# Kernel optimization log

Hardware: AMD Instinct MI355X
Metric: run time of the kernel (lower is better)

## Reference

```python
import jax, jax.numpy as jnp
import numpy as np

B, S, W, MODES, NUM, NLAYERS = 32, 8192, 128, 16, 8, 4
LG = 8192 + 40 - 1  # szie + len - 1 (Gabor filter length)
PI = float(np.pi)


def setup_inputs() -> dict:
    key = jax.random.key(0)
    ks = jax.random.split(key, 10)
    scale = 1.0 / (W * W)
    return {
        "x": jax.random.normal(ks[0], (B, S, 1), jnp.float32),
        "w1_re": scale * jax.random.uniform(ks[1], (NLAYERS, W, W, MODES), jnp.float32),
        "w1_im": scale * jax.random.uniform(ks[2], (NLAYERS, W, W, MODES), jnp.float32),
        "gamma": jnp.tile(jnp.linspace(0.01, 0.02, NUM, dtype=jnp.float32)[None], (NLAYERS, 1)),
        "fwhm": jnp.tile(jnp.linspace(0.001, 0.002, NUM, dtype=jnp.float32)[None], (NLAYERS, 1)),
        "w2": jax.random.uniform(ks[3], (NLAYERS, NUM), jnp.float32),
        "cw": jax.random.normal(ks[4], (NLAYERS, W, W), jnp.float32) / np.sqrt(W),
        "cb": jnp.zeros((NLAYERS, W), jnp.float32),
        "fc0_w": jax.random.normal(ks[5], (W, 2), jnp.float32) / np.sqrt(2.0),
        "fc0_b": jnp.zeros((W,), jnp.float32),
        "fc1_w": jax.random.normal(ks[6], (128, W), jnp.float32) / np.sqrt(W),
        "fc1_b": jnp.zeros((128,), jnp.float32),
        "fc2_w": jax.random.normal(ks[7], (1, 128), jnp.float32) / np.sqrt(128.0),
        "fc2_b": jnp.zeros((1,), jnp.float32),
    }


def _spectral_conv(h, w_re, w_im, gamma, fwhm, w2):
    # h: [B, C, S] real. w_re/w_im: [C, C, MODES]. gamma/fwhm/w2: [NUM].
    u = jnp.linspace(-0.5, 0.5, LG, dtype=h.dtype)                      # [LG]
    t1 = (gamma * PI / (fwhm + 1e-5))[:, None]                          # [NUM,1]
    gab = jnp.exp(-(t1 ** 2) * (u[None, :] - fwhm[:, None]) ** 2)       # [NUM,LG]
    gab = jnp.fft.ifftshift(gab, axes=-1)[:, :MODES]                     # [NUM,MODES]
    # weights2 is a scalar per latent kernel -> fold the num-reduction into an
    # effective per-mode Gabor weight (exact same math as the repeated einsum + sum).
    g_eff = jnp.einsum("k,km->m", w2, gab)                               # [MODES]
    w1 = (w_re + 1j * w_im) * g_eff[None, None, :]                       # [C,C,MODES] complex
    xf = jnp.fft.rfft(h)                                                 # [B,C,F], F=S//2+1
    out_m = jnp.einsum("bim,iom->bom", xf[..., :MODES], w1)              # [B,C,MODES]
    out = jnp.zeros(xf.shape, dtype=xf.dtype).at[..., :MODES].set(out_m)
    return jnp.fft.irfft(out, n=h.shape[-1])                             # [B,C,S]


def reference(x, w1_re, w1_im, gamma, fwhm, w2, cw, cb, fc0_w, fc0_b, fc1_w, fc1_b, fc2_w, fc2_b):
    b, s, _ = x.shape
    grid = jnp.broadcast_to(jnp.linspace(0.0, 1.0, s, dtype=x.dtype)[None, :, None], (b, s, 1))
    h = jnp.concatenate([x, grid], axis=-1)                              # [B,S,2]
    h = h @ fc0_w.T + fc0_b                                              # [B,S,W]
    h = jnp.transpose(h, (0, 2, 1))                                      # [B,W,S]
    for l in range(NLAYERS):
        x1 = _spectral_conv(h, w1_re[l], w1_im[l], gamma[l], fwhm[l], w2[l])
        x2 = jnp.einsum("oi,bis->bos", cw[l], h) + cb[l][None, :, None]  # 1x1 conv
        h = x1 + x2
        if l < NLAYERS - 1:
            h = jax.nn.gelu(h, approximate=False)
    h = jnp.transpose(h, (0, 2, 1))                                      # [B,S,W]
    h = jax.nn.gelu(h @ fc1_w.T + fc1_b, approximate=False)              # [B,S,128]
    return h @ fc2_w.T + fc2_b                                           # [B,S,1]
```

## Files before the change

kernel.cpp:

```cpp
#include <hip/hip_runtime.h>
#include <hip/hip_fp16.h>

#define BB 32
#define SS 8192
#define CC 128
#define MM 16
#define NUMK 8
#define NL 4

#define TWO_PI 6.2831853071795864769f

typedef _Float16 f16x8 __attribute__((ext_vector_type(8)));
typedef float f32x4 __attribute__((ext_vector_type(4)));

#define MFMA16(a, b, c) __builtin_amdgcn_mfma_f32_16x16x32_f16((a), (b), (c), 0, 0, 0)

__device__ __forceinline__ float gelu_f(float v) {
    float u = 0.7978845608f * fmaf(0.044715f * v * v, v, v);
    float a = fabsf(u);
    float e = __expf(-2.0f * a);
    float th = __fdividef(1.0f - e, 1.0f + e);
    th = copysignf(th, u);
    return 0.5f * v * (1.0f + th);
}

__device__ __align__(256) __half g_trigA[SS * 32];
__device__ __align__(256) __half g_trigD[32 * SS];
__device__ __align__(256) __half g_cwh[NL * CC * CC];
__device__ __align__(256) __half g_fc1h[CC * CC];
__device__ __align__(256) __half g_omh[BB * CC * 32];
__device__ __align__(256) float  g_Xfp[BB * 64 * 32 * CC];
__device__ __align__(256) float  g_Xf[BB * 32 * CC];
__device__ __align__(256) float  g_Xx[BB * MM * 2];
__device__ __align__(256) float  g_Xg[MM * 2];

__global__ __launch_bounds__(256) void k_prep(const float* __restrict__ cw,
                                              const float* __restrict__ fc1_w) {
    int idx = blockIdx.x * 256 + threadIdx.x;
    if (idx < NL * CC * CC) g_cwh[idx] = __float2half(cw[idx]);
    if (idx < CC * CC)      g_fc1h[idx] = __float2half(fc1_w[idx]);
}

__global__ __launch_bounds__(256) void k_trig() {
    int s = blockIdx.x * 256 + threadIdx.x;
    for (int m = 0; m < MM; m++) {
        int ms = (m * s) & (SS - 1);
        float th = (float)ms * (TWO_PI / (float)SS);
        float sn, cs;
        sincosf(th, &sn, &cs);
        g_trigA[s * 32 + m]        = __float2half(cs);
        g_trigA[s * 32 + 16 + m]   = __float2half(sn);
        g_trigD[m * SS + s]        = __float2half(cs);
        g_trigD[(16 + m) * SS + s] = __float2half(-sn);
    }
}

__global__ __launch_bounds__(256) void k_dftx(const float* __restrict__ x) {
    __shared__ float red[4][MM][2];
    int blk = blockIdx.x;
    int t = threadIdx.x;
    int lane = t & 63;
    int wv = t >> 6;

    float accR[MM], accI[MM], cr[MM], ci[MM], pc[MM], ps[MM];
#pragma unroll
    for (int m = 0; m < MM; m++) {
        float sn, cs;
        sincosf((TWO_PI / (float)SS) * (float)(m * t), &sn, &cs);
        cr[m] = cs; ci[m] = -sn;
        sincosf((TWO_PI * 256.0f / (float)SS) * (float)m, &sn, &cs);
        pc[m] = cs; ps[m] = -sn;
        accR[m] = 0.f; accI[m] = 0.f;
    }
    for (int k = 0; k < 32; k++) {
        int s = t + (k << 8);
        float v = (blk < BB) ? x[(blk << 13) + s] : (float)s * (1.0f / 8191.0f);
#pragma unroll
        for (int m = 0; m < MM; m++) {
            accR[m] = fmaf(v, cr[m], accR[m]);
            accI[m] = fmaf(v, ci[m], accI[m]);
            float nc = cr[m] * pc[m] - ci[m] * ps[m];
            float ns = cr[m] * ps[m] + ci[m] * pc[m];
            cr[m] = nc; ci[m] = ns;
        }
    }
#pragma unroll
    for (int m = 0; m < MM; m++) {
#pragma unroll
        for (int off = 32; off > 0; off >>= 1) {
            accR[m] += __shfl_xor(accR[m], off, 64);
            accI[m] += __shfl_xor(accI[m], off, 64);
        }
        if (lane == 0) { red[wv][m][0] = accR[m]; red[wv][m][1] = accI[m]; }
    }
    __syncthreads();
    if (t < MM * 2) {
        int m = t >> 1, p = t & 1;
        float s = red[0][m][p] + red[1][m][p] + red[2][m][p] + red[3][m][p];
        if (blk < BB) g_Xx[(blk << 5) + (m << 1) + p] = s;
        else          g_Xg[(m << 1) + p] = s;
    }
}

__global__ __launch_bounds__(256) void k_xf0(const float* __restrict__ fc0_w,
                                             const float* __restrict__ fc0_b) {
    int n = blockIdx.x * 256 + threadIdx.x;
    int i = n & 127, m2 = (n >> 7) & 31, b = n >> 12;
    int m = m2 & 15, p = m2 >> 4;
    float xv = g_Xx[(b << 5) + (m << 1) + p];
    float gv = g_Xg[(m << 1) + p];
    float v = fc0_w[2 * i] * xv + fc0_w[2 * i + 1] * gv;
    if (p == 0 && m == 0) v += (float)SS * fc0_b[i];
    g_Xf[(b << 12) + (m2 << 7) + i] = v;
}

__global__ __launch_bounds__(256) void k_fc0(const float* __restrict__ x,
                                             const float* __restrict__ fc0_w,
                                             const float* __restrict__ fc0_b,
                                             __half* __restrict__ h) {
    int idx = blockIdx.x * 256 + threadIdx.x;
    int wq = idx & 15;
    int s = (idx >> 4) & (SS - 1);
    int b = idx >> 17;
    float g = (float)s * (1.0f / (float)(SS - 1));
    float xv = x[(b << 13) + s];
    union { __half2 q[4]; f16x8 v; } pk;
#pragma unroll
    for (int j = 0; j < 4; j++) {
        int w = wq * 8 + j * 2;
        float4 fw = *(const float4*)(fc0_w + 2 * w);
        float2 fb = *(const float2*)(fc0_b + w);
        float v0 = fmaf(fw.x, xv, fmaf(fw.y, g, fb.x));
        float v1 = fmaf(fw.z, xv, fmaf(fw.w, g, fb.y));
        pk.q[j] = __floats2half2_rn(v0, v1);
    }
    *(f16x8*)((char*)h + ((long)idx << 4)) = pk.v;
}

__global__ __launch_bounds__(256) void k_red2() {
    int n = blockIdx.x * 256 + threadIdx.x;
    int i = n & 127, m2 = (n >> 7) & 31, b = n >> 12;
    const float* p = g_Xfp + (((b << 6) << 5) + (m2 << 7)) + i;
    float s = 0.f;
#pragma unroll 8
    for (int t = 0; t < 64; t++) s += p[t << 12];
    g_Xf[(b << 12) + (m2 << 7) + i] = s;
}

__global__ __launch_bounds__(256) void k_mix(const float* __restrict__ w1_re,
                                             const float* __restrict__ w1_im,
                                             const float* __restrict__ gamma,
                                             const float* __restrict__ fwhm,
                                             const float* __restrict__ w2,
                                             const float* __restrict__ cb, int l) {
    __shared__ float geff[MM];
    int t = threadIdx.x;
    if (t < MM) {
        float g = 0.f;
        for (int k = 0; k < NUMK; k++) {
            float fw = fwhm[l * NUMK + k];
            float t1 = gamma[l * NUMK + k] * 3.14159265358979f / (fw + 1e-5f);
            float u = (float)t * (1.0f / 8230.0f) - fw;
            g = fmaf(w2[l * NUMK + k], expf(-t1 * t1 * u * u), g);
        }
        geff[t] = g;
    }
    __syncthreads();

    int n = blockIdx.x * 256 + t;
    int m = n & 15, o = (n >> 4) & 127, b = n >> 11;
    const float* xr = g_Xf + (b << 12) + (m << 7);
    const float* xi = g_Xf + (b << 12) + ((16 + m) << 7);
    const float* wr = w1_re + (l << 18) + (o << 4) + m;
    const float* wi = w1_im + (l << 18) + (o << 4) + m;
    float orr = 0.f, oii = 0.f;
    for (int i = 0; i < CC; i++) {
        float xrv = xr[i], xiv = xi[i];
        float wrv = wr[i << 11], wiv = wi[i << 11];
        orr = fmaf(xrv, wrv, orr); orr = fmaf(-xiv, wiv, orr);
        oii = fmaf(xrv, wiv, oii); oii = fmaf(xiv, wrv, oii);
    }
    float sc = geff[m] * (2.0f / (float)SS) * ((m == 0) ? 0.5f : 1.0f);
    float base = (m == 0) ? cb[l * CC + o] : 0.0f;
    g_omh[(b << 12) + (o << 5) + m]      = __float2half(orr * sc + base);
    g_omh[(b << 12) + (o << 5) + 16 + m] = __float2half(-oii * sc);
}

#define GEMM_STEP(KS, HA, HB)                                                       \
    _Pragma("unroll")                                                               \
    for (int af = 0; af < 8; af++) {                                                \
        int row = (af << 4) + lr;                                                   \
        const f16x8 av = *(const f16x8*)(ldsA + (row << 8) +                        \
                          ((((KS << 2) + lg) ^ (row & 7)) << 4));                   \
        acc[af][0] = MFMA16(av, HA, acc[af][0]);                                    \
        acc[af][1] = MFMA16(av, HB, acc[af][1]);                                    \
    }

#define LOAD_HF(S0X)                                                                \
    {                                                                               \
        int hr = (((b << 13) + (S0X) + (wid << 5) + lr) << 8) + (lg << 4);          \
        hf0 = *(const f16x8*)(h_c + hr);                                            \
        hf1 = *(const f16x8*)(h_c + hr + (16 << 8));                                \
        hf2 = *(const f16x8*)(h_c + hr + (1 << 6));                                 \
        hf3 = *(const f16x8*)(h_c + hr + (16 << 8) + (1 << 6));                     \
        hf4 = *(const f16x8*)(h_c + hr + (2 << 6));                                 \
        hf5 = *(const f16x8*)(h_c + hr + (16 << 8) + (2 << 6));                     \
        hf6 = *(const f16x8*)(h_c + hr + (3 << 6));                                 \
        hf7 = *(const f16x8*)(h_c + hr + (16 << 8) + (3 << 6));                     \
    }

#define LOAD_TF(S0X)                                                                \
    {                                                                               \
        int tr2 = (((S0X) + (wid << 5) + lr) << 6) + (lg << 4);                     \
        tf0 = *(const f16x8*)(ta_c + tr2);                                          \
        tf1 = *(const f16x8*)(ta_c + tr2 + (16 << 6));                              \
    }

__global__ __launch_bounds__(256, 2) void k_layer(__half* __restrict__ h, int l) {
    __shared__ __align__(16) char smem[73728];
    char* ldsA = smem;
    char* ldsO = smem + 32768;
    char* ldsS = smem + 40960;
    int bi = blockIdx.x;
    int b = bi >> 4, grp = bi & 15;
    int Sg = grp << 9;
    int t = threadIdx.x;
    int wid = __builtin_amdgcn_readfirstlane(t >> 6);
    int l6 = t & 63, lr = l6 & 15, lg = l6 >> 4;
    const char* h_c = (const char*)h;
    char* hw = (char*)h;
    const char* cw_c = (const char*)(g_cwh + l * CC * CC);
    const char* om_c = (const char*)(g_omh + (b << 12));
    const char* ta_c = (const char*)g_trigA;
    const char* td_c = (const char*)g_trigD;
    char* strip = ldsS + (wid << 13);

#pragma unroll
    for (int k = 0; k < 8; k++) {
        int c = (k << 8) + t;
        f16x8 v = *(const f16x8*)(cw_c + (c << 4));
        int row = c >> 4, c16 = c & 15;
        *(f16x8*)(ldsA + (row << 8) + ((c16 ^ (row & 7)) << 4)) = v;
    }
#pragma unroll
    for (int k = 0; k < 2; k++) {
        int c = (k << 8) + t;
        f16x8 v = *(const f16x8*)(om_c + (c << 4));
        int row = c >> 2, c4 = c & 3;
        *(f16x8*)(ldsO + (row << 6) + ((c4 ^ (row & 3)) << 4)) = v;
    }
    f16x8 hf0, hf1, hf2, hf3, hf4, hf5, hf6, hf7, tf0, tf1;
    LOAD_HF(Sg)
    LOAD_TF(Sg)
    __syncthreads();

    f32x4 dacc[8][2];
#pragma unroll
    for (int af = 0; af < 8; af++) {
        dacc[af][0] = (f32x4){0.f, 0.f, 0.f, 0.f};
        dacc[af][1] = (f32x4){0.f, 0.f, 0.f, 0.f};
    }

    for (int ti = 0; ti < 4; ti++) {
        int S0 = Sg + (ti << 7);
        f32x4 acc[8][2];
#pragma unroll
        for (int af = 0; af < 8; af++) {
            acc[af][0] = (f32x4){0.f, 0.f, 0.f, 0.f};
            acc[af][1] = (f32x4){0.f, 0.f, 0.f, 0.f};
        }
        __builtin_amdgcn_s_setprio(1);
        GEMM_STEP(0, hf0, hf1)
        GEMM_STEP(1, hf2, hf3)
        GEMM_STEP(2, hf4, hf5)
        GEMM_STEP(3, hf6, hf7)
#pragma unroll
        for (int af = 0; af < 8; af++) {
            int row = (af << 4) + lr;
            const f16x8 ov = *(const f16x8*)(ldsO + (row << 6) + ((lg ^ (row & 3)) << 4));
            acc[af][0] = MFMA16(ov, tf0, acc[af][0]);
            acc[af][1] = MFMA16(ov, tf1, acc[af][1]);
        }
        __builtin_amdgcn_s_setprio(0);
        if (ti < 3) {
            int S0n = S0 + 128;
            LOAD_HF(S0n)
            LOAD_TF(S0n)
        }
        f16x8 td0, td1;
        {
            int sgl = S0 + (wid << 5) + (lg << 3);
            td0 = *(const f16x8*)(td_c + (((lr << 13) + sgl) << 1));
            td1 = *(const f16x8*)(td_c + ((((16 + lr) << 13) + sgl) << 1));
        }
#pragma unroll
        for (int bf = 0; bf < 2; bf++) {
            int s_w = (bf << 4) + lr;
#pragma unroll
            for (int af = 0; af < 8; af++) {
                int o0 = (af << 4) + (lg << 2);
                float v0 = gelu_f(acc[af][bf][0]), v1 = gelu_f(acc[af][bf][1]);
                float v2 = gelu_f(acc[af][bf][2]), v3 = gelu_f(acc[af][bf][3]);
                union { __half2 q[2]; unsigned long long u; } pk;
                pk.q[0] = __floats2half2_rn(v0, v1);
                pk.q[1] = __floats2half2_rn(v2, v3);
                int byte = (s_w << 8) + ((o0 << 1) ^ ((s_w & 15) << 4));
                *(unsigned long long*)(strip + byte) = pk.u;
            }
        }
        asm volatile("s_waitcnt lgkmcnt(0)" ::: "memory");
        __builtin_amdgcn_sched_barrier(0);
#pragma unroll
        for (int af = 0; af < 8; af++) {
            int o = (af << 4) + lr;
            union { unsigned int u[4]; f16x8 v; } bb;
#pragma unroll
            for (int p = 0; p < 4; p++) {
                int s0 = (lg << 3) + 2 * p, s1 = s0 + 1;
                unsigned int lo = *(const unsigned short*)
                    (strip + (s0 << 8) + ((o << 1) ^ ((s0 & 15) << 4)));
                unsigned int hi = *(const unsigned short*)
                    (strip + (s1 << 8) + ((o << 1) ^ ((s1 & 15) << 4)));
                bb.u[p] = lo | (hi << 16);
            }
            dacc[af][0] = MFMA16(td0, bb.v, dacc[af][0]);
            dacc[af][1] = MFMA16(td1, bb.v, dacc[af][1]);
        }
#pragma unroll
        for (int rg = 0; rg < 8; rg++) {
            int s_w = (rg << 2) + lg;
            f16x8 rd = *(const f16x8*)(strip + (s_w << 8) + ((lr ^ (s_w & 15)) << 4));
            *(f16x8*)(hw + (((b << 13) + S0 + (wid << 5) + s_w) << 8) + (lr << 4)) = rd;
        }
    }
    {
        float* xp = g_Xfp + (((b << 6) + (grp << 2) + wid) << 12);
#pragma unroll
        for (int af = 0; af < 8; af++)
#pragma unroll
            for (int mh = 0; mh < 2; mh++)
#pragma unroll
                for (int reg = 0; reg < 4; reg++) {
                    int m2 = (mh << 4) + (lg << 2) + reg;
                    int o = (af << 4) + lr;
                    xp[(m2 << 7) + o] = dacc[af][mh][reg];
                }
    }
}

__global__ __launch_bounds__(256, 2) void k_tail(const __half* __restrict__ h,
                                                 const float* __restrict__ fc1_b,
                                                 const float* __restrict__ fc2_w,
                                                 const float* __restrict__ fc2_b,
                                                 float* __restrict__ out) {
    __shared__ __align__(16) char smem[73728];
    char* ldsA = smem;
    char* ldsO = smem + 32768;
    char* ldsS = smem + 40960;
    int bi = blockIdx.x;
    int b = bi >> 4, grp = bi & 15;
    int Sg = grp << 9;
    int t = threadIdx.x;
    int wid = __builtin_amdgcn_readfirstlane(t >> 6);
    int l6 = t & 63, lr = l6 & 15, lg = l6 >> 4;
    const char* h_c = (const char*)h;
    const char* cw_c = (const char*)(g_cwh + 3 * CC * CC);
    const char* om_c = (const char*)(g_omh + (b << 12));
    const char* ta_c = (const char*)g_trigA;
    const char* f1_c = (const char*)g_fc1h;
    char* strip = ldsS + (wid << 13);

#pragma unroll
    for (int k = 0; k < 8; k++) {
        int c = (k << 8) + t;
        f16x8 v = *(const f16x8*)(cw_c + (c << 4));
        int row = c >> 4, c16 = c & 15;
        *(f16x8*)(ldsA + (row << 8) + ((c16 ^ (row & 7)) << 4)) = v;
    }
#pragma unroll
    for (int k = 0; k < 2; k++) {
        int c = (k << 8) + t;
        f16x8 v = *(const f16x8*)(om_c + (c << 4));
        int row = c >> 2, c4 = c & 3;
        *(f16x8*)(ldsO + (row << 6) + ((c4 ^ (row & 3)) << 4)) = v;
    }
    f16x8 hf0, hf1, hf2, hf3, hf4, hf5, hf6, hf7, tf0, tf1;
    LOAD_HF(Sg)
    LOAD_TF(Sg)
    __syncthreads();

    float f2b = fc2_b[0];
    for (int ti = 0; ti < 4; ti++) {
        int S0 = Sg + (ti << 7);
        {
            f32x4 acc[8][2];
#pragma unroll
            for (int af = 0; af < 8; af++) {
                acc[af][0] = (f32x4){0.f, 0.f, 0.f, 0.f};
                acc[af][1] = (f32x4){0.f, 0.f, 0.f, 0.f};
            }
            __builtin_amdgcn_s_setprio(1);
            GEMM_STEP(0, hf0, hf1)
            GEMM_STEP(1, hf2, hf3)
            GEMM_STEP(2, hf4, hf5)
            GEMM_STEP(3, hf6, hf7)
#pragma unroll
            for (int af = 0; af < 8; af++) {
                int row = (af << 4) + lr;
                const f16x8 ov = *(const f16x8*)(ldsO + (row << 6) + ((lg ^ (row & 3)) << 4));
                acc[af][0] = MFMA16(ov, tf0, acc[af][0]);
                acc[af][1] = MFMA16(ov, tf1, acc[af][1]);
            }
            __builtin_amdgcn_s_setprio(0);
            if (ti < 3) {
                int S0n = S0 + 128;
                LOAD_HF(S0n)
                LOAD_TF(S0n)
            }
#pragma unroll
            for (int bf = 0; bf < 2; bf++) {
                int s_w = (bf << 4) + lr;
#pragma unroll
                for (int af = 0; af < 8; af++) {
                    int o0 = (af << 4) + (lg << 2);
                    union { __half2 q[2]; unsigned long long u; } pk;
                    pk.q[0] = __floats2half2_rn(acc[af][bf][0], acc[af][bf][1]);
                    pk.q[1] = __floats2half2_rn(acc[af][bf][2], acc[af][bf][3]);
                    int byte = (s_w << 8) + ((o0 << 1) ^ ((s_w & 15) << 4));
                    *(unsigned long long*)(strip + byte) = pk.u;
                }
            }
        }
        asm volatile("s_waitcnt lgkmcnt(0)" ::: "memory");
        __builtin_amdgcn_sched_barrier(0);
        {
            f32x4 acc2[8][2];
#pragma unroll
            for (int af = 0; af < 8; af++) {
                acc2[af][0] = (f32x4){0.f, 0.f, 0.f, 0.f};
                acc2[af][1] = (f32x4){0.f, 0.f, 0.f, 0.f};
            }
#pragma unroll
            for (int ks = 0; ks < 4; ks++) {
#pragma unroll
                for (int bf = 0; bf < 2; bf++) {
                    int s_loc = (bf << 4) + lr;
                    union { unsigned int u[4]; f16x8 v; } bb;
#pragma unroll
                    for (int p = 0; p < 4; p++) {
                        int o0 = (ks << 5) + (lg << 3) + 2 * p, o1 = o0 + 1;
                        unsigned int lo = *(const unsigned short*)
                            (strip + (s_loc << 8) + ((o0 << 1) ^ ((s_loc & 15) << 4)));
                        unsigned int hi = *(const unsigned short*)
                            (strip + (s_loc << 8) + ((o1 << 1) ^ ((s_loc & 15) << 4)));
                        bb.u[p] = lo | (hi << 16);
                    }
#pragma unroll
                    for (int af = 0; af < 8; af++) {
                        const f16x8 av = *(const f16x8*)
                            (f1_c + (((af << 4) + lr) << 8) + (ks << 6) + (lg << 4));
                        acc2[af][bf] = MFMA16(av, bb.v, acc2[af][bf]);
                    }
                }
            }
            float p[2] = {0.f, 0.f};
#pragma unroll
            for (int af = 0; af < 8; af++) {
                float4 fb = *(const float4*)(fc1_b + (af << 4) + (lg << 2));
                float4 f2 = *(const float4*)(fc2_w + (af << 4) + (lg << 2));
#pragma unroll
                for (int bf = 0; bf < 2; bf++) {
                    float v0 = gelu_f(acc2[af][bf][0] + fb.x);
                    float v1 = gelu_f(acc2[af][bf][1] + fb.y);
                    float v2 = gelu_f(acc2[af][bf][2] + fb.z);
                    float v3 = gelu_f(acc2[af][bf][3] + fb.w);
                    p[bf] += f2.x * v0 + f2.y * v1 + f2.z * v2 + f2.w * v3;
                }
            }
#pragma unroll
            for (int bf = 0; bf < 2; bf++) {
                float v = p[bf];
                v += __shfl_xor(v, 16, 64);
                v += __shfl_xor(v, 32, 64);
                if (lg == 0) out[(b << 13) + S0 + (wid << 5) + (bf << 4) + lr] = v + f2b;
            }
        }
    }
}

extern "C" void kernel_launch(void* const* d_in, const int* in_sizes, int n_in,
                              void* d_out, int out_size, void* d_ws, size_t ws_size,
                              hipStream_t stream) {
    const float* x      = (const float*)d_in[0];
    const float* w1_re  = (const float*)d_in[1];
    const float* w1_im  = (const float*)d_in[2];
    const float* gamma  = (const float*)d_in[3];
    const float* fwhm   = (const float*)d_in[4];
    const float* w2     = (const float*)d_in[5];
    const float* cw     = (const float*)d_in[6];
    const float* cb     = (const float*)d_in[7];
    const float* fc0_w  = (const float*)d_in[8];
    const float* fc0_b  = (const float*)d_in[9];
    const float* fc1_w  = (const float*)d_in[10];
    const float* fc1_b  = (const float*)d_in[11];
    const float* fc2_w  = (const float*)d_in[12];
    const float* fc2_b  = (const float*)d_in[13];
    float* out = (float*)d_out;

    __half* h = (__half*)d_ws;

    k_prep<<<dim3(256), dim3(256), 0, stream>>>(cw, fc1_w);
    k_trig<<<dim3(32), dim3(256), 0, stream>>>();
    k_dftx<<<dim3(33), dim3(256), 0, stream>>>(x);
    k_xf0<<<dim3(512), dim3(256), 0, stream>>>(fc0_w, fc0_b);
    k_fc0<<<dim3(16384), dim3(256), 0, stream>>>(x, fc0_w, fc0_b, h);
    for (int l = 0; l < NL; l++) {
        k_mix<<<dim3(256), dim3(256), 0, stream>>>(w1_re, w1_im, gamma, fwhm, w2, cb, l);
        if (l < NL - 1) {
            k_layer<<<dim3(512), dim3(256), 0, stream>>>(h, l);
            k_red2<<<dim3(512), dim3(256), 0, stream>>>();
        } else {
            k_tail<<<dim3(512), dim3(256), 0, stream>>>(h, fc1_b, fc2_w, fc2_b, out);
        }
    }
}
```

Measured before the change: 372.3 us.

## Fuse fc0 lift into first layer kernel and reduce DFT partials in-block

Removes the standalone fc0 kernel, which wrote the full lifted activation to global memory. The first layer now recomputes the lift on the fly from x and the grid using half-precision FMAs, via a template flag. The spectral partial sums are reduced across the four waves through shared memory before writing, so the partial buffer and the k_red2 loop shrink by a factor of four. The activation write-back is also moved from a strip re-read to direct global stores of the packed outputs. This trades extra syncthreads and smaller, scattered stores for less global traffic, and computing the lift in fp16 may change numerics slightly.

```diff
diff --git a/kernel.cpp b/kernel.cpp
--- a/kernel.cpp
+++ b/kernel.cpp
@@ -29,7 +29,7 @@
 __device__ __align__(256) __half g_cwh[NL * CC * CC];
 __device__ __align__(256) __half g_fc1h[CC * CC];
 __device__ __align__(256) __half g_omh[BB * CC * 32];
-__device__ __align__(256) float  g_Xfp[BB * 64 * 32 * CC];
+__device__ __align__(256) float  g_Xfp[BB * 16 * 32 * CC];
 __device__ __align__(256) float  g_Xf[BB * 32 * CC];
 __device__ __align__(256) float  g_Xx[BB * MM * 2];
 __device__ __align__(256) float  g_Xg[MM * 2];
@@ -114,36 +114,13 @@
     g_Xf[(b << 12) + (m2 << 7) + i] = v;
 }
 
-__global__ __launch_bounds__(256) void k_fc0(const float* __restrict__ x,
-                                             const float* __restrict__ fc0_w,
-                                             const float* __restrict__ fc0_b,
-                                             __half* __restrict__ h) {
-    int idx = blockIdx.x * 256 + threadIdx.x;
-    int wq = idx & 15;
-    int s = (idx >> 4) & (SS - 1);
-    int b = idx >> 17;
-    float g = (float)s * (1.0f / (float)(SS - 1));
-    float xv = x[(b << 13) + s];
-    union { __half2 q[4]; f16x8 v; } pk;
-#pragma unroll
-    for (int j = 0; j < 4; j++) {
-        int w = wq * 8 + j * 2;
-        float4 fw = *(const float4*)(fc0_w + 2 * w);
-        float2 fb = *(const float2*)(fc0_b + w);
-        float v0 = fmaf(fw.x, xv, fmaf(fw.y, g, fb.x));
-        float v1 = fmaf(fw.z, xv, fmaf(fw.w, g, fb.y));
-        pk.q[j] = __floats2half2_rn(v0, v1);
-    }
-    *(f16x8*)((char*)h + ((long)idx << 4)) = pk.v;
-}
-
 __global__ __launch_bounds__(256) void k_red2() {
     int n = blockIdx.x * 256 + threadIdx.x;
     int i = n & 127, m2 = (n >> 7) & 31, b = n >> 12;
-    const float* p = g_Xfp + (((b << 6) << 5) + (m2 << 7)) + i;
+    const float* p = g_Xfp + ((long)b << 16) + (m2 << 7) + i;
     float s = 0.f;
 #pragma unroll 8
-    for (int t = 0; t < 64; t++) s += p[t << 12];
+    for (int t = 0; t < 16; t++) s += p[t << 12];
     g_Xf[(b << 12) + (m2 << 7) + i] = s;
 }
 
@@ -216,7 +193,11 @@
         tf1 = *(const f16x8*)(ta_c + tr2 + (16 << 6));                              \
     }
 
-__global__ __launch_bounds__(256, 2) void k_layer(__half* __restrict__ h, int l) {
+template <int SRC>
+__global__ __launch_bounds__(256, 2) void k_layer(__half* __restrict__ h,
+                                                  const float* __restrict__ x,
+                                                  const float* __restrict__ fc0_w,
+                                                  const float* __restrict__ fc0_b, int l) {
     __shared__ __align__(16) char smem[73728];
     char* ldsA = smem;
     char* ldsO = smem + 32768;
@@ -250,7 +231,34 @@
         *(f16x8*)(ldsO + (row << 6) + ((c4 ^ (row & 3)) << 4)) = v;
     }
     f16x8 hf0, hf1, hf2, hf3, hf4, hf5, hf6, hf7, tf0, tf1;
-    LOAD_HF(Sg)
+    union HU { __half2 q[4]; f16x8 v; };
+    HU c0[4], c1[4], cbh[4];
+    float xv0 = 0.f, xv1 = 0.f;
+    if (SRC) {
+#pragma unroll
+        for (int ks = 0; ks < 4; ks++) {
+            int i0 = (ks << 5) + (lg << 3);
+            const float* wp = fc0_w + (i0 << 1);
+            float4 a  = *(const float4*)(wp);
+            float4 bq = *(const float4*)(wp + 4);
+            float4 cq = *(const float4*)(wp + 8);
+            float4 dq = *(const float4*)(wp + 12);
+            c0[ks].q[0] = __floats2half2_rn(a.x, a.z);   c1[ks].q[0] = __floats2half2_rn(a.y, a.w);
+            c0[ks].q[1] = __floats2half2_rn(bq.x, bq.z); c1[ks].q[1] = __floats2half2_rn(bq.y, bq.w);
+            c0[ks].q[2] = __floats2half2_rn(cq.x, cq.z); c1[ks].q[2] = __floats2half2_rn(cq.y, cq.w);
+            c0[ks].q[3] = __floats2half2_rn(dq.x, dq.z); c1[ks].q[3] = __floats2half2_rn(dq.y, dq.w);
+            float4 e = *(const float4*)(fc0_b + i0);
+            float4 f = *(const float4*)(fc0_b + i0 + 4);
+            cbh[ks].q[0] = __floats2half2_rn(e.x, e.y);
+            cbh[ks].q[1] = __floats2half2_rn(e.z, e.w);
+            cbh[ks].q[2] = __floats2half2_rn(f.x, f.y);
+            cbh[ks].q[3] = __floats2half2_rn(f.z, f.w);
+        }
+        xv0 = x[(b << 13) + Sg + (wid << 5) + lr];
+        xv1 = x[(b << 13) + Sg + (wid << 5) + 16 + lr];
+    } else {
+        LOAD_HF(Sg)
+    }
     LOAD_TF(Sg)
     __syncthreads();
 
@@ -263,6 +271,28 @@
 
     for (int ti = 0; ti < 4; ti++) {
         int S0 = Sg + (ti << 7);
+        if (SRC) {
+            int sA = S0 + (wid << 5) + lr;
+            __half2 xx0 = __floats2half2_rn(xv0, xv0);
+            __half2 xx1 = __floats2half2_rn(xv1, xv1);
+            float gv0 = (float)sA * (1.0f / 8191.0f);
+            float gv1 = (float)(sA + 16) * (1.0f / 8191.0f);
+            __half2 gg0 = __floats2half2_rn(gv0, gv0);
+            __half2 gg1 = __floats2half2_rn(gv1, gv1);
+#pragma unroll
+            for (int ks = 0; ks < 4; ks++) {
+                HU r0, r1;
+#pragma unroll
+                for (int q = 0; q < 4; q++) {
+                    r0.q[q] = __hfma2(c0[ks].q[q], xx0, __hfma2(c1[ks].q[q], gg0, cbh[ks].q[q]));
+                    r1.q[q] = __hfma2(c0[ks].q[q], xx1, __hfma2(c1[ks].q[q], gg1, cbh[ks].q[q]));
+                }
+                if (ks == 0)      { hf0 = r0.v; hf1 = r1.v; }
+                else if (ks == 1) { hf2 = r0.v; hf3 = r1.v; }
+                else if (ks == 2) { hf4 = r0.v; hf5 = r1.v; }
+                else              { hf6 = r0.v; hf7 = r1.v; }
+            }
+        }
         f32x4 acc[8][2];
 #pragma unroll
         for (int af = 0; af < 8; af++) {
@@ -284,7 +314,12 @@
         __builtin_amdgcn_s_setprio(0);
         if (ti < 3) {
             int S0n = S0 + 128;
-            LOAD_HF(S0n)
+            if (SRC) {
+                xv0 = x[(b << 13) + S0n + (wid << 5) + lr];
+                xv1 = x[(b << 13) + S0n + (wid << 5) + 16 + lr];
+            } else {
+                LOAD_HF(S0n)
+            }
             LOAD_TF(S0n)
         }
         f16x8 td0, td1;
@@ -296,6 +331,7 @@
 #pragma unroll
         for (int bf = 0; bf < 2; bf++) {
             int s_w = (bf << 4) + lr;
+            int s = S0 + (wid << 5) + s_w;
 #pragma unroll
             for (int af = 0; af < 8; af++) {
                 int o0 = (af << 4) + (lg << 2);
@@ -304,6 +340,7 @@
                 union { __half2 q[2]; unsigned long long u; } pk;
                 pk.q[0] = __floats2half2_rn(v0, v1);
                 pk.q[1] = __floats2half2_rn(v2, v3);
+                *(unsigned long long*)(hw + (((b << 13) + s) << 8) + (o0 << 1)) = pk.u;
                 int byte = (s_w << 8) + ((o0 << 1) ^ ((s_w & 15) << 4));
                 *(unsigned long long*)(strip + byte) = pk.u;
             }
@@ -326,25 +363,58 @@
             dacc[af][0] = MFMA16(td0, bb.v, dacc[af][0]);
             dacc[af][1] = MFMA16(td1, bb.v, dacc[af][1]);
         }
-#pragma unroll
-        for (int rg = 0; rg < 8; rg++) {
-            int s_w = (rg << 2) + lg;
-            f16x8 rd = *(const f16x8*)(strip + (s_w << 8) + ((lr ^ (s_w & 15)) << 4));
-            *(f16x8*)(hw + (((b << 13) + S0 + (wid << 5) + s_w) << 8) + (lr << 4)) = rd;
-        }
     }
     {
-        float* xp = g_Xfp + (((b << 6) + (grp << 2) + wid) << 12);
-#pragma unroll
-        for (int af = 0; af < 8; af++)
-#pragma unroll
-            for (int mh = 0; mh < 2; mh++)
-#pragma unroll
-                for (int reg = 0; reg < 4; reg++) {
-                    int m2 = (mh << 4) + (lg << 2) + reg;
-                    int o = (af << 4) + lr;
-                    xp[(m2 << 7) + o] = dacc[af][mh][reg];
-                }
+        float* red = (float*)ldsS;
+        __syncthreads();
+        if (wid == 1 || wid == 3) {
+            float* rp = red + ((wid >> 1) << 12) + l6;
+#pragma unroll
+            for (int af = 0; af < 8; af++)
+#pragma unroll
+                for (int mh = 0; mh < 2; mh++)
+#pragma unroll
+                    for (int reg = 0; reg < 4; reg++)
+                        rp[((af << 3) + (mh << 2) + reg) << 6] = dacc[af][mh][reg];
+        }
+        __syncthreads();
+        if (wid == 0 || wid == 2) {
+            const float* rp = red + ((wid >> 1) << 12) + l6;
+#pragma unroll
+            for (int af = 0; af < 8; af++)
+#pragma unroll
+                for (int mh = 0; mh < 2; mh++)
+#pragma unroll
+                    for (int reg = 0; reg < 4; reg++)
+                        dacc[af][mh][reg] += rp[((af << 3) + (mh << 2) + reg) << 6];
+        }
+        __syncthreads();
+        if (wid == 2) {
+            float* rp = red + l6;
+#pragma unroll
+            for (int af = 0; af < 8; af++)
+#pragma unroll
+                for (int mh = 0; mh < 2; mh++)
+#pragma unroll
+                    for (int reg = 0; reg < 4; reg++)
+                        rp[((af << 3) + (mh << 2) + reg) << 6] = dacc[af][mh][reg];
+        }
+        __syncthreads();
+        if (wid == 0) {
+            const float* rp = red + l6;
+            float* xp = g_Xfp + (((long)(b << 4) + grp) << 12);
+#pragma unroll
+            for (int af = 0; af < 8; af++)
+#pragma unroll
+                for (int mh = 0; mh < 2; mh++)
+#pragma unroll
+                    for (int reg = 0; reg < 4; reg++) {
+                        float v = dacc[af][mh][reg] + rp[((af << 3) + (mh << 2) + reg) << 6];
+                        int m2 = (mh << 4) + (lg << 2) + reg;
+                        int o = (af << 4) + lr;
+                        xp[(m2 << 7) + o] = v;
+                    }
+        }
     }
 }
 
@@ -513,11 +583,13 @@
     k_trig<<<dim3(32), dim3(256), 0, stream>>>();
     k_dftx<<<dim3(33), dim3(256), 0, stream>>>(x);
     k_xf0<<<dim3(512), dim3(256), 0, stream>>>(fc0_w, fc0_b);
-    k_fc0<<<dim3(16384), dim3(256), 0, stream>>>(x, fc0_w, fc0_b, h);
     for (int l = 0; l < NL; l++) {
         k_mix<<<dim3(256), dim3(256), 0, stream>>>(w1_re, w1_im, gamma, fwhm, w2, cb, l);
-        if (l < NL - 1) {
-            k_layer<<<dim3(512), dim3(256), 0, stream>>>(h, l);
+        if (l == 0) {
+            k_layer<1><<<dim3(512), dim3(256), 0, stream>>>(h, x, fc0_w, fc0_b, l);
+            k_red2<<<dim3(512), dim3(256), 0, stream>>>();
+        } else if (l < NL - 1) {
+            k_layer<0><<<dim3(512), dim3(256), 0, stream>>>(h, x, fc0_w, fc0_b, l);
             k_red2<<<dim3(512), dim3(256), 0, stream>>>();
         } else {
             k_tail<<<dim3(512), dim3(256), 0, stream>>>(h, fc1_b, fc2_w, fc2_b, out);
```

Measured after the change: 312.5 us. 16.1% less time.
